# Kernel optimization log

Hardware: AMD Instinct MI355X
Metric: run time of the kernel (lower is better)

Reference implementation:

```python
import jax, jax.numpy as jnp
import numpy as np

K = 5          # kernel_size per dim
B = 100        # batch size (hard-coded in source)
GRID = 28
NUM_FIRST_FC = 49  # adjs[2].size(0) = 7*7


def spline_conv(x, edge_index, pseudo, W, root, bias):
    """Degree-1 open B-spline graph conv (SplineGCN).
    x: [N, Cin]; edge_index: [2, E] (src, dst); pseudo: [E, 2] in [0,1];
    W: [K*K, Cin, Cout]; root: [Cin, Cout]; bias: [Cout].
    out_i = mean_{j->i} sum_taps b_tap(u_ij) * (x_j @ W[k_tap]) + x_i @ root + bias
    """
    N = x.shape[0]
    src, dst = edge_index[0], edge_index[1]
    pos = pseudo * (K - 1)                     # open spline: scale to [0, K-1]
    kf = jnp.floor(pos)
    frac = pos - kf                            # [E, 2]
    k0 = kf.astype(jnp.int32)
    k1 = jnp.minimum(k0 + 1, K - 1)
    # Precompute x @ W[k] for all 25 kernel indices: [N, K*K, Cout]
    y = jnp.einsum('ni,kio->nko', x, W)
    fx, fy = frac[:, 0], frac[:, 1]
    taps = [
        (k0[:, 0], k0[:, 1], (1 - fx) * (1 - fy)),
        (k0[:, 0], k1[:, 1], (1 - fx) * fy),
        (k1[:, 0], k0[:, 1], fx * (1 - fy)),
        (k1[:, 0], k1[:, 1], fx * fy),
    ]
    msg = jnp.zeros((src.shape[0], W.shape[2]), dtype=x.dtype)
    for ax, ay, w in taps:
        msg = msg + w[:, None] * y[src, ax * K + ay]   # gather [E, Cout]
    agg = jax.ops.segment_sum(msg, dst, num_segments=N)
    deg = jax.ops.segment_sum(jnp.ones_like(msg[:, 0]), dst, num_segments=N)
    return agg / jnp.maximum(deg, 1.0)[:, None] + x @ root + bias


def max_pool2(x):  # x: [b, H, W, C] -> [b, H/2, W/2, C] (same math as NCHW pool)
    b, h, w, c = x.shape
    return x.reshape(b, h // 2, 2, w // 2, 2, c).max(axis=(2, 4))


def setup_inputs() -> dict:
    key = jax.random.key(0)
    ks = jax.random.split(key, 16)
    N0, N1 = B * GRID * GRID, B * (GRID // 2) * (GRID // 2)
    E0, E1 = N0 * 8, N1 * 8
    s = 0.1
    return {
        'x': jax.random.normal(ks[0], (N0, 1), dtype=jnp.float32),
        'pseudo0': jax.random.uniform(ks[1], (E0, 2), dtype=jnp.float32),
        'pseudo1': jax.random.uniform(ks[2], (E1, 2), dtype=jnp.float32),
        'W1': jax.random.normal(ks[3], (K * K, 1, 32), dtype=jnp.float32) * s,
        'root1': jax.random.normal(ks[4], (1, 32), dtype=jnp.float32) * s,
        'b1': jnp.zeros((32,), dtype=jnp.float32),
        'W2': jax.random.normal(ks[5], (K * K, 32, 64), dtype=jnp.float32) * s,
        'root2': jax.random.normal(ks[6], (32, 64), dtype=jnp.float32) * s,
        'b2': jnp.zeros((64,), dtype=jnp.float32),
        'fc1_w': jax.random.normal(ks[7], (NUM_FIRST_FC * 64, 512), dtype=jnp.float32) * 0.02,
        'fc1_b': jnp.zeros((512,), dtype=jnp.float32),
        'fc2_w': jax.random.normal(ks[8], (512, 10), dtype=jnp.float32) * 0.02,
        'fc2_b': jnp.zeros((10,), dtype=jnp.float32),
        'edge_index0': jax.random.randint(ks[9], (2, E0), 0, N0, dtype=jnp.int32),
        'edge_index1': jax.random.randint(ks[10], (2, E1), 0, N1, dtype=jnp.int32),
    }


def reference(x, pseudo0, pseudo1, W1, root1, b1, W2, root2, b2,
              fc1_w, fc1_b, fc2_w, fc2_b, edge_index0, edge_index1):
    elu = jax.nn.elu
    # conv1 on 28x28 grid graph
    h = elu(spline_conv(x, edge_index0, pseudo0, W1, root1, b1))   # [B*784, 32]
    h = h.reshape(-1, GRID, GRID, 32)                              # [B, 28, 28, 32]
    h = max_pool2(h)                                               # [B, 14, 14, 32]
    h = h.reshape(-1, 32)                                          # [B*196, 32]
    # conv2 on 14x14 grid graph
    h = elu(spline_conv(h, edge_index1, pseudo1, W2, root2, b2))   # [B*196, 64]
    # faithful replication of the source's reshapes: (B*196) rows -> (B/4, 28, 28, 64)
    h = h.reshape(-1, GRID, GRID, 64)                              # [25, 28, 28, 64]
    h = max_pool2(h)                                               # [25, 14, 14, 64]
    h = h.reshape(-1, NUM_FIRST_FC * 64)                           # [100, 3136]
    h = elu(h @ fc1_w + fc1_b)
    # F.dropout with training=False (eval) is identity
    h = elu(h @ fc2_w + fc2_b)
    return jax.nn.log_softmax(h, axis=-1)
```

## Files before the change

### kernel.cpp

```cpp
#include <hip/hip_runtime.h>
#include <hip/hip_bf16.h>

#define KK 5
constexpr int N0 = 78400;
constexpr int E0 = 627200;
constexpr int N1 = 19600;
constexpr int E1 = 156800;
constexpr int C1 = 32, C2 = 64;
constexpr int BSZ = 100;
constexpr int FC1_IN = 3136, FC1_OUT = 512;
constexpr int NKEYS = 98000;
constexpr int NCOARSE = 383;
constexpr int CAPB = 2400;
constexpr int KEXT = 832;
constexpr int ULS = 836;
constexpr int UBS = 856;
constexpr int CH2 = 192;
constexpr int CH1 = 640;
constexpr int KZ = 7;

typedef __attribute__((ext_vector_type(8))) short bf16x8;
typedef __attribute__((ext_vector_type(4))) float f32x4;

__device__ __forceinline__ unsigned short f2bf(float f) {
    union { float f; unsigned u; } v; v.f = f;
    unsigned u = v.u;
    unsigned r = (u + 0x7FFF + ((u >> 16) & 1)) >> 16;
    return (unsigned short)r;
}

__device__ __forceinline__ void taps4(float px, float py,
                                      int& a00, int& a01, int& a10, int& a11,
                                      float& fx, float& fy) {
    float kfx = floorf(px), kfy = floorf(py);
    fx = px - kfx; fy = py - kfy;
    int k0x = min(max((int)kfx, 0), KK - 1);
    int k0y = min(max((int)kfy, 0), KK - 1);
    int k1x = min(k0x + 1, KK - 1), k1y = min(k0y + 1, KK - 1);
    a00 = k0x * KK + k0y; a01 = k0x * KK + k1y;
    a10 = k1x * KK + k0y; a11 = k1x * KK + k1y;
}

__global__ void coarse_bin(const int* __restrict__ ei0, const int* __restrict__ ei1,
                           const float* __restrict__ ps0, const float* __restrict__ ps1,
                           int* __restrict__ gcur, int2* __restrict__ pk2,
                           const float* __restrict__ fc1w, const float* __restrict__ W2,
                           const float* __restrict__ root2,
                           unsigned short* __restrict__ wt1,
                           unsigned short* __restrict__ w2t) {
    __shared__ int hist[NCOARSE];
    __shared__ int gbase[NCOARSE];
    __shared__ unsigned short tile[64 * 66];
    int t = threadIdx.x;
    if (blockIdx.x >= 192) {
        int pb = blockIdx.x - 192;
        if (pb >= 392) {
            int base = (pb - 392) * 6656;
            for (int i2 = t; i2 < 6656; i2 += 512) {
                int idx = base + i2;
                int o = idx / KEXT, k = idx - o * KEXT;
                float v = (k < 800) ? W2[k * 64 + o] : root2[(k - 800) * 64 + o];
                w2t[idx] = f2bf(v);
            }
            return;
        }
        int k0 = (pb >> 3) * 64, j0 = (pb & 7) * 64;
        int jj = t & 63, ks = t >> 6;
        for (int kk = ks; kk < 64; kk += 8)
            tile[kk * 66 + jj] = f2bf(fc1w[(k0 + kk) * FC1_OUT + j0 + jj]);
        __syncthreads();
        int kk2 = t & 63, js = t >> 6;
        for (int j2 = js; j2 < 64; j2 += 8)
            wt1[(j0 + j2) * FC1_IN + k0 + kk2] = tile[kk2 * 66 + j2];
        return;
    }
    for (int i = t; i < NCOARSE; i += 512) hist[i] = 0;
    __syncthreads();
    int e0b = blockIdx.x * 4096;
    int keys[8], rnk[8], pay0[8], pay1[8];
#pragma unroll
    for (int j = 0; j < 8; j++) {
        int e = e0b + t + j * 512;
        int gk = -1, p0 = 0, p1v = 0;
        if (e < E0) {
            gk = ei0[E0 + e];
            float px = ps0[2 * e] * 4.f, py = ps0[2 * e + 1] * 4.f;
            unsigned ux = min((unsigned)(px * 16384.f + 0.5f), 65535u);
            unsigned uy = min((unsigned)(py * 16384.f + 0.5f), 65535u);
            p0 = ei0[e]; p1v = (int)(ux | (uy << 16));
        } else if (e < E0 + E1) {
            int el = e - E0;
            gk = N0 + ei1[E1 + el];
            float px = ps1[2 * el] * 4.f, py = ps1[2 * el + 1] * 4.f;
            unsigned ux = min((unsigned)(px * 16384.f + 0.5f), 65535u);
            unsigned uy = min((unsigned)(py * 16384.f + 0.5f), 65535u);
            p0 = ei1[el]; p1v = (int)(ux | (uy << 16));
        }
        keys[j] = gk; pay0[j] = p0; pay1[j] = p1v;
    }
#pragma unroll
    for (int j = 0; j < 8; j++)
        if (keys[j] >= 0) rnk[j] = atomicAdd(&hist[keys[j] >> 8], 1);
    __syncthreads();
    for (int i = t; i < NCOARSE; i += 512)
        gbase[i] = hist[i] ? atomicAdd(&gcur[i], hist[i]) : 0;
    __syncthreads();
#pragma unroll
    for (int j = 0; j < 8; j++) {
        if (keys[j] >= 0) {
            int b = keys[j] >> 8;
            int p = gbase[b] + rnk[j];
            if (p < CAPB)
                pk2[b * CAPB + p] = make_int2(pay0[j] | ((keys[j] & 255) << 20), pay1[j]);
        }
    }
}

__global__ void fine_sort(const int2* __restrict__ pk2, const int* __restrict__ gcur,
                          int2* __restrict__ erec, int* __restrict__ off) {
    __shared__ int cl[NCOARSE];
    __shared__ int2 ent[CAPB];
    __shared__ int rnk[CAPB];
    __shared__ int h2[256];
    __shared__ int sc[256];
    __shared__ int redbuf[4];
    __shared__ int baseS;
    int b = blockIdx.x, t = threadIdx.x;
    for (int i2 = t; i2 < NCOARSE; i2 += 256) cl[i2] = min(gcur[i2], CAPB);
    __syncthreads();
    {
        int s = 0;
        if (t < b) s += cl[t];
        if (t + 256 < b) s += cl[t + 256];
#pragma unroll
        for (int o2 = 32; o2 > 0; o2 >>= 1) s += __shfl_down(s, o2);
        if ((t & 63) == 0) redbuf[t >> 6] = s;
        __syncthreads();
        if (t == 0) baseS = redbuf[0] + redbuf[1] + redbuf[2] + redbuf[3];
        __syncthreads();
    }
    int base = baseS;
    int cb = cl[b];
    h2[t] = 0;
    __syncthreads();
    for (int i = t; i < cb; i += 256) {
        int2 v = pk2[b * CAPB + i];
        ent[i] = v;
        rnk[i] = atomicAdd(&h2[(v.x >> 20) & 255], 1);
    }
    __syncthreads();
    int v0 = h2[t];
    sc[t] = v0;
    __syncthreads();
    for (int d = 1; d < 256; d <<= 1) {
        int add = (t >= d) ? sc[t - d] : 0;
        __syncthreads();
        sc[t] += add;
        __syncthreads();
    }
    int excl = sc[t] - v0;
    __syncthreads();
    sc[t] = excl;
    __syncthreads();
    int n = (b << 8) + t;
    if (n < NKEYS) off[n] = base + excl;
    if (b == 0 && t == 0) off[NKEYS] = E0 + E1;
    for (int i = t; i < cb; i += 256) {
        int2 v = ent[i];
        erec[base + sc[(v.x >> 20) & 255] + rnk[i]] = v;
    }
}

__global__ __launch_bounds__(256, 4)
void conv1_pool(const int2* __restrict__ erec, const int* __restrict__ off,
                const float* __restrict__ x,
                const float* __restrict__ W1,
                const float* __restrict__ root, const float* __restrict__ bias,
                float* __restrict__ p1) {
    __shared__ float S4[224 * 25];
    __shared__ float Sr[56 * 25];
    __shared__ float exv[CH1], efx[CH1], efy[CH1];
    __shared__ int   emt[CH1];
    float* h1t = S4;
    int t = threadIdx.x;
    int bb = blockIdx.x;
    int n0 = bb * 56;
    int q = t & 3, nl = t >> 2;
    bool actN = nl < 56;
    int n = n0 + (actN ? nl : 0);
    float* sp = S4 + (actN ? (nl * 4 + q) : 0) * 25;
    for (int i = t; i < 224 * 25; i += 256) S4[i] = 0.f;
    int e0 = off[n0], e1 = off[n0 + 56];
    int my0 = off[n], my1 = off[n + 1];
    for (int base = e0; base < e1; base += CH1) {
        int nE = min(e1 - base, CH1);
        __syncthreads();
        for (int j = t; j < nE; j += 256) {
            int2 r = erec[base + j];
            int src = r.x & 0xFFFFF;
            float px = (float)((unsigned)r.y & 0xFFFF) * (1.f / 16384.f);
            float py = (float)((unsigned)r.y >> 16) * (1.f / 16384.f);
            int a00, a01, a10, a11; float fx, fy;
            taps4(px, py, a00, a01, a10, a11, fx, fy);
            emt[j] = a00 | (a01 << 5) | (a10 << 10) | (a11 << 15);
            efx[j] = fx; efy[j] = fy;
            exv[j] = x[src];
        }
        __syncthreads();
        if (actN) {
            int r0 = max(my0 - base, 0), r1 = min(my1 - base, nE);
            for (int p = r0 + q; p < r1; p += 4) {
                float xv = exv[p]; int m = emt[p];
                float fx = efx[p], fy = efy[p];
                float gx = 1.f - fx, gy = 1.f - fy;
                sp[m & 31]         += gx * gy * xv;
                sp[(m >> 5) & 31]  += gx * fy * xv;
                sp[(m >> 10) & 31] += fx * gy * xv;
                sp[(m >> 15) & 31] += fx * fy * xv;
            }
        }
    }
    __syncthreads();
    for (int i2 = t; i2 < 56 * 25; i2 += 256) {
        int n2 = i2 / 25, a = i2 - n2 * 25;
        Sr[i2] = S4[(n2 * 4 + 0) * 25 + a] + S4[(n2 * 4 + 1) * 25 + a] +
                 S4[(n2 * 4 + 2) * 25 + a] + S4[(n2 * 4 + 3) * 25 + a];
    }
    __syncthreads();
    {
        int o = t & 31, ng = t >> 5;
        float w1c[25];
#pragma unroll
        for (int a = 0; a < 25; a++) w1c[a] = W1[a * C1 + o];
        float ro = root[o], bo = bias[o];
        for (int j2 = 0; j2 < 7; j2++) {
            int nl2 = ng * 7 + j2;
            int n2 = n0 + nl2;
            float acc = 0.f;
#pragma unroll
            for (int a = 0; a < 25; a++) acc += Sr[nl2 * 25 + a] * w1c[a];
            float invd = 1.f / fmaxf((float)(off[n2 + 1] - off[n2]), 1.f);
            float v = acc * invd + x[n2] * ro + bo;
            h1t[nl2 * 32 + o] = v > 0.f ? v : expm1f(v);
        }
    }
    __syncthreads();
    for (int i2 = t; i2 < 448; i2 += 256) {
        int o2 = i2 & 31, pc = i2 >> 5;
        float m0 = h1t[(2 * pc) * 32 + o2],      m1 = h1t[(2 * pc + 1) * 32 + o2];
        float m2 = h1t[(28 + 2 * pc) * 32 + o2], m3 = h1t[(28 + 2 * pc + 1) * 32 + o2];
        p1[(bb * 14 + pc) * C1 + o2] = fmaxf(fmaxf(m0, m1), fmaxf(m2, m3));
    }
}

__global__ __launch_bounds__(512, 4)
void conv2_fused(const float* __restrict__ p1, const int2* __restrict__ erec,
                 const int* __restrict__ off,
                 const unsigned short* __restrict__ w2t,
                 const float* __restrict__ b2, float* __restrict__ h2) {
    __shared__ float Ul[16 * ULS];
    __shared__ int   es[CH2];
    __shared__ int   et[CH2];
    __shared__ float efx[CH2], efy[CH2];
    unsigned short* Ub = (unsigned short*)Ul;
    int t = threadIdx.x;
    int nb = blockIdx.x * 16;
    int i = t & 31;
    int g = t >> 5;
    float* up = Ul + g * ULS;
#pragma unroll
    for (int a = 0; a < 25; a++) up[a * 32 + i] = 0.f;
    up[800 + i] = p1[(nb + g) * C1 + i];
    int e0 = off[N0 + nb], e1 = off[N0 + nb + 16];
    int my0 = off[N0 + nb + g], my1 = off[N0 + nb + g + 1];
    for (int base = e0; base < e1; base += CH2) {
        int nE = min(e1 - base, CH2);
        __syncthreads();
        for (int j = t; j < nE; j += 512) {
            int2 r = erec[base + j];
            es[j] = r.x & 0xFFFFF;
            float px = (float)((unsigned)r.y & 0xFFFF) * (1.f / 16384.f);
            float py = (float)((unsigned)r.y >> 16) * (1.f / 16384.f);
            int a00, a01, a10, a11; float fx, fy;
            taps4(px, py, a00, a01, a10, a11, fx, fy);
            et[j] = a00 | (a01 << 5) | (a10 << 10) | (a11 << 15);
            efx[j] = fx; efy[j] = fy;
        }
        __syncthreads();
        int r0 = max(my0 - base, 0);
        int r1 = min(my1 - base, nE);
        int cnt = max(r1 - r0, 0);
        int m4 = max(cnt, __shfl_xor(cnt, 32));
        for (int jj = 0; jj < m4; jj += 4) {
            bool a0 = jj < cnt, a1 = jj + 1 < cnt, a2 = jj + 2 < cnt, a3 = jj + 3 < cnt;
            int j0 = a0 ? r0 + jj     : 0;
            int j1 = a1 ? r0 + jj + 1 : 0;
            int j2 = a2 ? r0 + jj + 2 : 0;
            int j3 = a3 ? r0 + jj + 3 : 0;
            int s0 = es[j0], s1 = es[j1], s2 = es[j2], s3 = es[j3];
            int mm0 = et[j0], mm1 = et[j1], mm2 = et[j2], mm3 = et[j3];
            float fx0 = efx[j0], fy0 = efy[j0];
            float fx1 = efx[j1], fy1 = efy[j1];
            float fx2 = efx[j2], fy2 = efy[j2];
            float fx3 = efx[j3], fy3 = efy[j3];
            float x0 = p1[s0 * C1 + i];
            float x1 = p1[s1 * C1 + i];
            float x2 = p1[s2 * C1 + i];
            float x3 = p1[s3 * C1 + i];
            if (a0) {
                float gx = 1.f - fx0, gy = 1.f - fy0;
                up[(mm0 & 31) * 32 + i]         += gx * gy * x0;
                up[((mm0 >> 5) & 31) * 32 + i]  += gx * fy0 * x0;
                up[((mm0 >> 10) & 31) * 32 + i] += fx0 * gy * x0;
                up[((mm0 >> 15) & 31) * 32 + i] += fx0 * fy0 * x0;
            }
            if (a1) {
                float gx = 1.f - fx1, gy = 1.f - fy1;
                up[(mm1 & 31) * 32 + i]         += gx * gy * x1;
                up[((mm1 >> 5) & 31) * 32 + i]  += gx * fy1 * x1;
                up[((mm1 >> 10) & 31) * 32 + i] += fx1 * gy * x1;
                up[((mm1 >> 15) & 31) * 32 + i] += fx1 * fy1 * x1;
            }
            if (a2) {
                float gx = 1.f - fx2, gy = 1.f - fy2;
                up[(mm2 & 31) * 32 + i]         += gx * gy * x2;
                up[((mm2 >> 5) & 31) * 32 + i]  += gx * fy2 * x2;
                up[((mm2 >> 10) & 31) * 32 + i] += fx2 * gy * x2;
                up[((mm2 >> 15) & 31) * 32 + i] += fx2 * fy2 * x2;
            }
            if (a3) {
                float gx = 1.f - fx3, gy = 1.f - fy3;
                up[(mm3 & 31) * 32 + i]         += gx * gy * x3;
                up[((mm3 >> 5) & 31) * 32 + i]  += gx * fy3 * x3;
                up[((mm3 >> 10) & 31) * 32 + i] += fx3 * gy * x3;
                up[((mm3 >> 15) & 31) * 32 + i] += fx3 * fy3 * x3;
            }
        }
    }
    __syncthreads();
    {
        int g2 = t >> 5, i2c = t & 31;
        int dgc = off[N0 + nb + g2 + 1] - off[N0 + nb + g2];
        float invd = 1.f / fmaxf((float)dgc, 1.f);
        const float* srcp = Ul + g2 * ULS + i2c * 26;
        float rv[26];
#pragma unroll
        for (int j = 0; j < 26; j++) {
            float v = srcp[j];
            rv[j] = (i2c * 26 + j < 800) ? v * invd : v;
        }
        __syncthreads();
        unsigned* dstp = (unsigned*)(Ub + g2 * UBS + i2c * 26);
#pragma unroll
        for (int j = 0; j < 13; j++) {
            unsigned lo = f2bf(rv[2 * j]), hi = f2bf(rv[2 * j + 1]);
            dstp[j] = lo | (hi << 16);
        }
    }
    __syncthreads();
    int wv = t >> 6, lane = t & 63, quad = lane >> 4, lrow = lane & 15;
    if (wv < 4) {
        f32x4 acc = {0.f, 0.f, 0.f, 0.f};
        const unsigned short* bbase = w2t + (wv * 16 + lrow) * KEXT;
        const unsigned short* abase = Ub + lrow * UBS;
#pragma unroll
        for (int kc = 0; kc < 26; kc++) {
            bf16x8 a = *(const bf16x8*)(abase + kc * 32 + quad * 8);
            bf16x8 b = *(const bf16x8*)(bbase + kc * 32 + quad * 8);
            acc = __builtin_amdgcn_mfma_f32_16x16x32_bf16(a, b, acc, 0, 0, 0);
        }
        int o = wv * 16 + lrow;
        float bo = b2[o];
#pragma unroll
        for (int r = 0; r < 4; r++) {
            int node = quad * 4 + r;
            float v = acc[r] + bo;
            v = v > 0.f ? v : expm1f(v);
            h2[(nb + node) * C2 + o] = v;
        }
    }
}

__global__ void pool2b(const float* __restrict__ h2, unsigned short* __restrict__ p2b) {
    int idx = blockIdx.x * blockDim.x + threadIdx.x;
    if (idx >= 112 * FC1_IN) return;
    if (idx >= 100 * FC1_IN) { p2b[idx] = 0; return; }
    int o = idx & 63; int t2 = idx >> 6;
    int c = t2 % 14; int r = (t2 / 14) % 14; int b = t2 / 196;
    const float* base = h2 + (((b * 28 + 2 * r) * 28 + 2 * c) * C2 + o);
    float m = fmaxf(fmaxf(base[0], base[C2]),
                    fmaxf(base[28 * C2], base[28 * C2 + C2]));
    p2b[idx] = f2bf(m);
}

__global__ void gemm_fc1(const unsigned short* __restrict__ p2b,
                         const unsigned short* __restrict__ wt1,
                         float* __restrict__ z1p) {
    constexpr int AS = 232;
    __shared__ unsigned short as_[16 * AS];
    int t = threadIdx.x;
    int jt = blockIdx.x, mt = blockIdx.y, kz = blockIdx.z;
    int wv = t >> 6, lane = t & 63, quad = lane >> 4, lrow = lane & 15;
    int m0 = mt * 16;
    int kbase = kz * 448;
    const unsigned short* bbase = wt1 + (jt * 64 + wv * 16 + lrow) * FC1_IN + kbase;
    f32x4 acc = {0.f, 0.f, 0.f, 0.f};
    for (int ch = 0; ch < 2; ch++) {
        __syncthreads();
        for (int slot = t; slot < 448; slot += 256) {
            int r = slot / 28, c = slot - (slot / 28) * 28;
            *(uint4*)(as_ + r * AS + c * 8) =
                *(const uint4*)(p2b + (m0 + r) * FC1_IN + kbase + ch * 224 + c * 8);
        }
        __syncthreads();
        const unsigned short* ab = as_ + lrow * AS;
        const unsigned short* bb = bbase + ch * 224;
#pragma unroll
        for (int kk = 0; kk < 7; kk++) {
            bf16x8 a = *(const bf16x8*)(ab + kk * 32 + quad * 8);
            bf16x8 b = *(const bf16x8*)(bb + kk * 32 + quad * 8);
            acc = __builtin_amdgcn_mfma_f32_16x16x32_bf16(a, b, acc, 0, 0, 0);
        }
    }
    int n = jt * 64 + wv * 16 + lrow;
#pragma unroll
    for (int r = 0; r < 4; r++) {
        int m = m0 + quad * 4 + r;
        z1p[kz * (112 * FC1_OUT) + m * FC1_OUT + n] = acc[r];
    }
}

__global__ void fc2_lsm(const float* __restrict__ z1p, const float* __restrict__ fc1b,
                        const float* __restrict__ w, const float* __restrict__ fc2b,
                        float* __restrict__ out) {
    int b = blockIdx.x;
    int t = threadIdx.x;
    int wv = t >> 6;
    int lane = t & 63;
    float acc = 0.f;
#pragma unroll
    for (int m = 0; m < 8; m++) {
        int k = lane * 8 + m;
        float xv = fc1b[k];
#pragma unroll
        for (int p = 0; p < KZ; p++)
            xv += z1p[p * (112 * FC1_OUT) + b * FC1_OUT + k];
        xv = xv > 0.f ? xv : expm1f(xv);
        acc += xv * w[k * 10 + wv];
    }
#pragma unroll
    for (int off = 32; off > 0; off >>= 1) acc += __shfl_down(acc, off);
    __shared__ float zs[10];
    if (lane == 0) {
        float z = acc + fc2b[wv];
        zs[wv] = z > 0.f ? z : expm1f(z);
    }
    __syncthreads();
    if (t < 10) {
        float m = -1e30f;
        for (int jj = 0; jj < 10; jj++) m = fmaxf(m, zs[jj]);
        float s = 0.f;
        for (int jj = 0; jj < 10; jj++) s += expf(zs[jj] - m);
        out[b * 10 + t] = zs[t] - m - logf(s);
    }
}

extern "C" void kernel_launch(void* const* d_in, const int* in_sizes, int n_in,
                              void* d_out, int out_size, void* d_ws, size_t ws_size,
                              hipStream_t stream) {
    const float* x     = (const float*)d_in[0];
    const float* ps0   = (const float*)d_in[1];
    const float* ps1   = (const float*)d_in[2];
    const float* W1    = (const float*)d_in[3];
    const float* root1 = (const float*)d_in[4];
    const float* b1    = (const float*)d_in[5];
    const float* W2    = (const float*)d_in[6];
    const float* root2 = (const float*)d_in[7];
    const float* b2v   = (const float*)d_in[8];
    const float* fc1w  = (const float*)d_in[9];
    const float* fc1b  = (const float*)d_in[10];
    const float* fc2w  = (const float*)d_in[11];
    const float* fc2b  = (const float*)d_in[12];
    const int*   ei0   = (const int*)d_in[13];
    const int*   ei1   = (const int*)d_in[14];

    float* ws = (float*)d_ws;
    int*  gcur = (int*)ws;
    int*  off  = (int*)(ws + 384);
    int2* pk2  = (int2*)(ws + 98388);
    int2* erec = (int2*)(ws + 1936788);
    float* p1  = ws + 3504788;
    float* h2  = ws + 4131988;
    unsigned short* p2b = (unsigned short*)(ws + 5386388);
    float* z1p = ws + 5562004;
    unsigned short* w2t = (unsigned short*)(ws + 5963412);
    unsigned short* wt1 = (unsigned short*)(ws + 5990036);

    hipMemsetAsync(gcur, 0, (size_t)NCOARSE * sizeof(int), stream);

    coarse_bin<<<592, 512, 0, stream>>>(ei0, ei1, ps0, ps1, gcur, pk2,
                                        fc1w, W2, root2, wt1, w2t);
    fine_sort<<<NCOARSE, 256, 0, stream>>>(pk2, gcur, erec, off);
    conv1_pool<<<1400, 256, 0, stream>>>(erec, off, x, W1, root1, b1, p1);
    conv2_fused<<<N1 / 16, 512, 0, stream>>>(p1, erec, off, w2t, b2v, h2);
    pool2b<<<(112 * FC1_IN + 255) / 256, 256, 0, stream>>>(h2, p2b);
    gemm_fc1<<<dim3(8, 7, KZ), 256, 0, stream>>>(p2b, wt1, z1p);
    fc2_lsm<<<BSZ, 640, 0, stream>>>(z1p, fc1b, fc2w, fc2b, (float*)d_out);
}
```

Baseline: 202.5 us.

## Stage conv2 source-feature gathers into shared memory before per-node scatter

The conv2 edge loop previously gathered neighbor features from global memory inside each node's serial per-edge loop, unrolled by four with predication. Now all 16 warps cooperatively gather the chunk's source rows into a new shared buffer with four independent loads per warp, then each half-warp accumulates from shared memory in a simple loop. This is meant to spread gather latency evenly across warps and increase memory-level parallelism. In exchange it adds a barrier and about 20KB of LDS per block, which may reduce occupancy, and the chunk size shrinks to 160 to fit.

```diff
diff --git a/kernel.cpp b/kernel.cpp
--- a/kernel.cpp
+++ b/kernel.cpp
@@ -15,7 +15,7 @@
 constexpr int KEXT = 832;
 constexpr int ULS = 836;
 constexpr int UBS = 856;
-constexpr int CH2 = 192;
+constexpr int CH2 = 160;
 constexpr int CH1 = 640;
 constexpr int KZ = 7;
 
@@ -259,6 +259,7 @@
                  const unsigned short* __restrict__ w2t,
                  const float* __restrict__ b2, float* __restrict__ h2) {
     __shared__ float Ul[16 * ULS];
+    __shared__ float ev[CH2 * 32];
     __shared__ int   es[CH2];
     __shared__ int   et[CH2];
     __shared__ float efx[CH2], efy[CH2];
@@ -287,54 +288,34 @@
             efx[j] = fx; efy[j] = fy;
         }
         __syncthreads();
+        for (int j0 = g; j0 < nE; j0 += 64) {
+            int ja = j0, jb = j0 + 16, jc = j0 + 32, jd = j0 + 48;
+            bool vb = jb < nE, vc = jc < nE, vd = jd < nE;
+            int sa = es[ja];
+            int sb = vb ? es[jb] : sa;
+            int sc2 = vc ? es[jc] : sa;
+            int sd = vd ? es[jd] : sa;
+            float xa = p1[sa * C1 + i];
+            float xb = p1[sb * C1 + i];
+            float xc = p1[sc2 * C1 + i];
+            float xd = p1[sd * C1 + i];
+            ev[ja * 32 + i] = xa;
+            if (vb) ev[jb * 32 + i] = xb;
+            if (vc) ev[jc * 32 + i] = xc;
+            if (vd) ev[jd * 32 + i] = xd;
+        }
+        __syncthreads();
         int r0 = max(my0 - base, 0);
         int r1 = min(my1 - base, nE);
-        int cnt = max(r1 - r0, 0);
-        int m4 = max(cnt, __shfl_xor(cnt, 32));
-        for (int jj = 0; jj < m4; jj += 4) {
-            bool a0 = jj < cnt, a1 = jj + 1 < cnt, a2 = jj + 2 < cnt, a3 = jj + 3 < cnt;
-            int j0 = a0 ? r0 + jj     : 0;
-            int j1 = a1 ? r0 + jj + 1 : 0;
-            int j2 = a2 ? r0 + jj + 2 : 0;
-            int j3 = a3 ? r0 + jj + 3 : 0;
-            int s0 = es[j0], s1 = es[j1], s2 = es[j2], s3 = es[j3];
-            int mm0 = et[j0], mm1 = et[j1], mm2 = et[j2], mm3 = et[j3];
-            float fx0 = efx[j0], fy0 = efy[j0];
-            float fx1 = efx[j1], fy1 = efy[j1];
-            float fx2 = efx[j2], fy2 = efy[j2];
-            float fx3 = efx[j3], fy3 = efy[j3];
-            float x0 = p1[s0 * C1 + i];
-            float x1 = p1[s1 * C1 + i];
-            float x2 = p1[s2 * C1 + i];
-            float x3 = p1[s3 * C1 + i];
-            if (a0) {
-                float gx = 1.f - fx0, gy = 1.f - fy0;
-                up[(mm0 & 31) * 32 + i]         += gx * gy * x0;
-                up[((mm0 >> 5) & 31) * 32 + i]  += gx * fy0 * x0;
-                up[((mm0 >> 10) & 31) * 32 + i] += fx0 * gy * x0;
-                up[((mm0 >> 15) & 31) * 32 + i] += fx0 * fy0 * x0;
-            }
-            if (a1) {
-                float gx = 1.f - fx1, gy = 1.f - fy1;
-                up[(mm1 & 31) * 32 + i]         += gx * gy * x1;
-                up[((mm1 >> 5) & 31) * 32 + i]  += gx * fy1 * x1;
-                up[((mm1 >> 10) & 31) * 32 + i] += fx1 * gy * x1;
-                up[((mm1 >> 15) & 31) * 32 + i] += fx1 * fy1 * x1;
-            }
-            if (a2) {
-                float gx = 1.f - fx2, gy = 1.f - fy2;
-                up[(mm2 & 31) * 32 + i]         += gx * gy * x2;
-                up[((mm2 >> 5) & 31) * 32 + i]  += gx * fy2 * x2;
-                up[((mm2 >> 10) & 31) * 32 + i] += fx2 * gy * x2;
-                up[((mm2 >> 15) & 31) * 32 + i] += fx2 * fy2 * x2;
-            }
-            if (a3) {
-                float gx = 1.f - fx3, gy = 1.f - fy3;
-                up[(mm3 & 31) * 32 + i]         += gx * gy * x3;
-                up[((mm3 >> 5) & 31) * 32 + i]  += gx * fy3 * x3;
-                up[((mm3 >> 10) & 31) * 32 + i] += fx3 * gy * x3;
-                up[((mm3 >> 15) & 31) * 32 + i] += fx3 * fy3 * x3;
-            }
+        for (int p = r0; p < r1; p++) {
+            float xv = ev[p * 32 + i];
+            int m = et[p];
+            float fx = efx[p], fy = efy[p];
+            float gx = 1.f - fx, gy = 1.f - fy;
+            up[(m & 31) * 32 + i]         += gx * gy * xv;
+            up[((m >> 5) & 31) * 32 + i]  += gx * fy * xv;
+            up[((m >> 10) & 31) * 32 + i] += fx * gy * xv;
+            up[((m >> 15) & 31) * 32 + i] += fx * fy * xv;
         }
     }
     __syncthreads();
```

Measured after the change: 203.4 us. No clear change (+0.5%).
